# Kernel optimization log

Hardware: AMD Instinct MI355X
Metric: run time of the kernel (lower is better)

Reference implementation:

```python
import jax, jax.numpy as jnp
import numpy as np

MARGIN = 0.3
EPS = 1e-6  # torch pairwise_distance default eps used by TripletMarginLoss


def setup_inputs() -> dict:
    key = jax.random.key(0)
    k1, k2 = jax.random.split(key)
    emb = jax.random.normal(k1, (4096, 256), dtype=jnp.float32)
    emb = emb / jnp.linalg.norm(emb, axis=1, keepdims=True)  # docstring: normalized embeddings
    labels = jax.random.randint(k2, (4096,), 0, 64, dtype=jnp.int64) if jax.config.jax_enable_x64 else jax.random.randint(k2, (4096,), 0, 64, dtype=jnp.int32)
    return {"embeddings": emb, "labels": labels}


def _triplet_mining_loss(embeddings, labels):
    B = embeddings.shape[0]
    # pairwise euclidean distances via GEMM (matches torch.cdist p=2)
    sq = jnp.sum(embeddings * embeddings, axis=1)
    d2 = sq[:, None] + sq[None, :] - 2.0 * (embeddings @ embeddings.T)
    dist = jnp.sqrt(jnp.maximum(d2, 0.0))  # [B, B]

    same = labels[:, None] == labels[None, :]
    eye = jnp.eye(B, dtype=bool)
    pos_mask = same & ~eye
    neg_mask = ~same
    valid = pos_mask.any(axis=1) & neg_mask.any(axis=1)

    # hardest positive per anchor
    ap = jnp.where(pos_mask, dist, -jnp.inf)
    hp_idx = jnp.argmax(ap, axis=1)                           # [B]
    ap_dist = jnp.take_along_axis(dist, hp_idx[:, None], 1)[:, 0]

    # semi-hard negative: ap < d_an < ap + margin; pick FIRST such index (original takes semi_hard_indices[0])
    semi = neg_mask & (dist > ap_dist[:, None]) & (dist < ap_dist[:, None] + MARGIN)
    any_semi = semi.any(axis=1)
    first_semi = jnp.argmax(semi, axis=1)                     # argmax of bool = first True
    an = jnp.where(neg_mask, dist, jnp.inf)
    hardest_neg = jnp.argmin(an, axis=1)
    neg_idx = jnp.where(any_semi, first_semi, hardest_neg)

    # triplet margin loss recomputed from embeddings (torch adds EPS inside the norm)
    pos_e = embeddings[hp_idx]
    neg_e = embeddings[neg_idx]
    d_ap = jnp.linalg.norm(embeddings - pos_e + EPS, axis=1)
    d_an = jnp.linalg.norm(embeddings - neg_e + EPS, axis=1)
    per_anchor = jnp.maximum(d_ap - d_an + MARGIN, 0.0)

    vf = valid.astype(embeddings.dtype)
    cnt = jnp.sum(vf)
    return jnp.where(cnt > 0, jnp.sum(per_anchor * vf) / jnp.maximum(cnt, 1.0), 0.0)


def reference(embeddings, labels):
    return _triplet_mining_loss(embeddings, labels)
```

## Files before the change

### kernel.cpp

```cpp
#include <hip/hip_runtime.h>
#include <math.h>

#define BN 4096
#define DIM 256
#define D4 (DIM/4)
#define MI 8
#define MARGINF 0.3f
#define EPSF 1e-6f
#define SCAP 96
#define IMAX 0x7fffffff
#define PCAP 512

typedef __attribute__((ext_vector_type(8))) short bf16x8;
typedef __attribute__((ext_vector_type(4))) float f32x4;

__device__ __forceinline__ float fma4(float4 a, float4 b, float c){
  return fmaf(a.x,b.x, fmaf(a.y,b.y, fmaf(a.z,b.z, fmaf(a.w,b.w, c))));
}
__device__ __forceinline__ unsigned short f2bf(float x){
  unsigned u = __float_as_uint(x);
  return (unsigned short)((u + 0x7FFFu + ((u>>16)&1u)) >> 16);
}
__device__ __forceinline__ float bf2f(unsigned short h){
  return __uint_as_float(((unsigned)h)<<16);
}

__global__ __launch_bounds__(256) void k_pre2(const float* __restrict__ E,
     unsigned short* __restrict__ EhiT, unsigned short* __restrict__ EloT,
     float* __restrict__ sq, unsigned int* __restrict__ counter){
  int t = threadIdx.x;
  int g = blockIdx.x;
  const float4* E4 = (const float4*)E;
  bf16x8* HT = (bf16x8*)EhiT;
  bf16x8* LT = (bf16x8*)EloT;
  #pragma unroll
  for (int it=0; it<2; it++){
    int idx = it*256 + t;
    int kk = idx>>6, sub = idx&63, q = sub>>4, n = sub&15;
    int r = g*16 + n;
    int c = kk*4 + q;
    float4 v0 = E4[(size_t)r*64 + c*2];
    float4 v1 = E4[(size_t)r*64 + c*2 + 1];
    unsigned short h[8], lo[8];
    float vv[8] = {v0.x,v0.y,v0.z,v0.w, v1.x,v1.y,v1.z,v1.w};
    #pragma unroll
    for (int i=0;i<8;i++){ h[i]=f2bf(vv[i]); lo[i]=f2bf(vv[i]-bf2f(h[i])); }
    bf16x8 hv, lv;
    #pragma unroll
    for (int i=0;i<8;i++){ hv[i]=(short)h[i]; lv[i]=(short)lo[i]; }
    size_t d = (size_t)g*512 + idx;
    HT[d] = hv; LT[d] = lv;
  }
  int row = t>>4, part = t&15;
  const float4* rp = E4 + (size_t)(g*16+row)*64 + part*4;
  float s0 = fma4(rp[0],rp[0],0.f);
  float s1 = fma4(rp[1],rp[1],0.f);
  s0 = fma4(rp[2],rp[2],s0);
  s1 = fma4(rp[3],rp[3],s1);
  float s = s0+s1;
  s += __shfl_xor(s,1); s += __shfl_xor(s,2); s += __shfl_xor(s,4); s += __shfl_xor(s,8);
  if (part==0) sq[g*16+row] = s;
  if (g==0 && t==0) counter[0] = 0u;
}

__global__ __launch_bounds__(256) void k_posm(const float* __restrict__ E,
     const int* __restrict__ labels, const float* __restrict__ sq,
     float* __restrict__ apw, int* __restrict__ hpw,
     unsigned long long* __restrict__ negKey, unsigned int* __restrict__ semiJ){
  __shared__ __align__(16) int   labsS[BN];
  __shared__ __align__(16) float sqS[BN];
  __shared__ int mem[4][PCAP+4];
  int t=threadIdx.x, l=t&63, w=t>>6;
  #pragma unroll
  for (int i=0;i<4;i++){
    ((int4*)labsS)[i*256+t]   = ((const int4*)labels)[i*256+t];
    ((float4*)sqS)[i*256+t]   = ((const float4*)sq)[i*256+t];
  }
  __syncthreads();
  int aw = blockIdx.x*4 + w;
  int labW = labsS[aw];
  float sqw_ = sqS[aw];
  const float4* E4 = (const float4*)E;
  float4 areg = E4[(size_t)aw*64 + l];
  int cnt = 0;
  for (int c=0;c<64;c++){
    int j = c*64 + l;
    bool m = (labsS[j]==labW) && (j != aw);
    unsigned long long mask = __ballot(m);
    if (m){
      int pos = cnt + __popcll(mask & ((1ull<<l)-1ull));
      if (pos < PCAP) mem[w][pos] = j;
    }
    cnt += __popcll(mask);
  }
  if (cnt > PCAP) cnt = PCAP;
  if (l < 4) mem[w][cnt + l] = aw;
  float bv2 = -INFINITY; int bj = IMAX;
  for (int base=0; base<cnt; base+=4){
    int j0=mem[w][base+0], j1=mem[w][base+1], j2=mem[w][base+2], j3=mem[w][base+3];
    float4 r0=E4[(size_t)j0*64+l];
    float4 r1=E4[(size_t)j1*64+l];
    float4 r2=E4[(size_t)j2*64+l];
    float4 r3=E4[(size_t)j3*64+l];
    float p0=fma4(areg,r0,0.f), p1=fma4(areg,r1,0.f);
    float p2=fma4(areg,r2,0.f), p3=fma4(areg,r3,0.f);
    #pragma unroll
    for (int off=32; off; off>>=1){
      p0 += __shfl_xor(p0,off); p1 += __shfl_xor(p1,off);
      p2 += __shfl_xor(p2,off); p3 += __shfl_xor(p3,off);
    }
    float d0 = sqw_ + sqS[j0] - 2.0f*p0;
    float d1 = sqw_ + sqS[j1] - 2.0f*p1;
    float d2 = sqw_ + sqS[j2] - 2.0f*p2;
    float d3 = sqw_ + sqS[j3] - 2.0f*p3;
    if (d0 > bv2){ bv2=d0; bj=j0; }
    if (base+1<cnt && d1 > bv2){ bv2=d1; bj=j1; }
    if (base+2<cnt && d2 > bv2){ bv2=d2; bj=j2; }
    if (base+3<cnt && d3 > bv2){ bv2=d3; bj=j3; }
  }
  if (l==0){
    apw[aw] = (bj==IMAX) ? -INFINITY : sqrtf(fmaxf(bv2, 0.0f));
    hpw[aw] = (bj==IMAX) ? 0 : bj;
    negKey[aw] = ~0ull;
    semiJ[aw]  = 0xFFFFFFFFu;
  }
}

__global__ __launch_bounds__(1024,4) void k_negm(
     const unsigned short* __restrict__ EhiT, const unsigned short* __restrict__ EloT,
     const int* __restrict__ labels, const float* __restrict__ sq,
     const float* __restrict__ apw,
     unsigned long long* __restrict__ negKey, unsigned int* __restrict__ semiJ){
  __shared__ bf16x8 afH[1024];
  __shared__ bf16x8 afL[1024];
  __shared__ __align__(16) int   labsH[2048];
  __shared__ __align__(16) float sqH[2048];
  __shared__ float rnv[16][32]; __shared__ int rnj[16][32]; __shared__ int rsm[16][32];
  int t=threadIdx.x, l=t&63, w=t>>6;
  int lane16 = l&15, quad = l>>4;
  int q8   = blockIdx.x & 7;
  int half = q8 >> 2;
  int grp  = (blockIdx.x >> 3)*4 + (q8 & 3);
  int a0 = grp*32;
  int hbase = half*2048;
  const bf16x8* HT = (const bf16x8*)EhiT;
  const bf16x8* LT = (const bf16x8*)EloT;
  afH[t] = HT[(size_t)grp*1024 + t];
  afL[t] = LT[(size_t)grp*1024 + t];
  { int2   lv = ((const int2*)(labels + hbase))[t];
    labsH[2*t] = lv.x; labsH[2*t+1] = lv.y;
    float2 sv = ((const float2*)(sq + hbase))[t];
    sqH[2*t] = sv.x; sqH[2*t+1] = sv.y; }
  float sqa[2][4]; int laba[2][4]; float ap2[2][4]; float th2[2][4];
  #pragma unroll
  for (int g=0; g<2; g++){
    #pragma unroll
    for (int r=0; r<4; r++){
      int ag = a0 + g*16 + quad*4 + r;
      sqa[g][r] = sq[ag]; laba[g][r] = labels[ag];
      float ap = apw[ag];
      ap2[g][r] = ap*ap;
      float th = ap + MARGINF;
      th2[g][r] = th*th;
    }
  }
  __syncthreads();
  float mn[2][4]; int mj[2][4]; int sm[2][4];
  #pragma unroll
  for (int g=0; g<2; g++)
    #pragma unroll
    for (int r=0; r<4; r++){ mn[g][r]=INFINITY; mj[g][r]=IMAX; sm[g][r]=IMAX; }
  #pragma unroll 1
  for (int tile=0; tile<8; tile++){
    int gl = w*8 + tile;
    size_t BBase = (size_t)(half*128 + gl) * 512;
    f32x4 acc00={0.f,0.f,0.f,0.f}, acc01=acc00, acc02=acc00;
    f32x4 acc10=acc00, acc11=acc00, acc12=acc00;
    #pragma unroll 2
    for (int kk=0; kk<8; kk++){
      bf16x8 bh  = HT[BBase + kk*64 + l];
      bf16x8 bl  = LT[BBase + kk*64 + l];
      bf16x8 ah0 = afH[kk*64 + l];
      bf16x8 al0 = afL[kk*64 + l];
      bf16x8 ah1 = afH[512 + kk*64 + l];
      bf16x8 al1 = afL[512 + kk*64 + l];
      acc00 = __builtin_amdgcn_mfma_f32_16x16x32_bf16(ah0, bh, acc00, 0,0,0);
      acc01 = __builtin_amdgcn_mfma_f32_16x16x32_bf16(ah0, bl, acc01, 0,0,0);
      acc02 = __builtin_amdgcn_mfma_f32_16x16x32_bf16(al0, bh, acc02, 0,0,0);
      acc10 = __builtin_amdgcn_mfma_f32_16x16x32_bf16(ah1, bh, acc10, 0,0,0);
      acc11 = __builtin_amdgcn_mfma_f32_16x16x32_bf16(ah1, bl, acc11, 0,0,0);
      acc12 = __builtin_amdgcn_mfma_f32_16x16x32_bf16(al1, bh, acc12, 0,0,0);
    }
    int jloc = gl*16 + lane16;
    int lj = labsH[jloc]; float sqj = sqH[jloc];
    int jglob = hbase + jloc;
    #pragma unroll
    for (int r=0; r<4; r++){
      float dot0 = acc00[r] + (acc01[r] + acc02[r]);
      float d20  = sqa[0][r] + sqj - 2.0f*dot0;
      if (lj != laba[0][r]){
        if (d20 < mn[0][r]){ mn[0][r]=d20; mj[0][r]=jglob; }
        if (d20 > ap2[0][r] && d20 < th2[0][r] && jglob < sm[0][r]) sm[0][r]=jglob;
      }
      float dot1 = acc10[r] + (acc11[r] + acc12[r]);
      float d21  = sqa[1][r] + sqj - 2.0f*dot1;
      if (lj != laba[1][r]){
        if (d21 < mn[1][r]){ mn[1][r]=d21; mj[1][r]=jglob; }
        if (d21 > ap2[1][r] && d21 < th2[1][r] && jglob < sm[1][r]) sm[1][r]=jglob;
      }
    }
  }
  #pragma unroll
  for (int g=0; g<2; g++){
    #pragma unroll
    for (int r=0; r<4; r++){
      float v=mn[g][r]; int j=mj[g][r]; int s=sm[g][r];
      #pragma unroll
      for (int off=1; off<16; off<<=1){
        float v2=__shfl_xor(v,off); int j2=__shfl_xor(j,off); int s2=__shfl_xor(s,off);
        if (v2<v || (v2==v && j2<j)){ v=v2; j=j2; }
        s = (s2<s)?s2:s;
      }
      if (lane16==0){
        int ai = g*16 + quad*4 + r;
        rnv[w][ai]=v; rnj[w][ai]=j; rsm[w][ai]=s;
      }
    }
  }
  __syncthreads();
  if (t < 32){
    float V=INFINITY; int J=IMAX; int S=IMAX;
    for (int q=0; q<16; q++){
      float v2=rnv[q][t]; int j2=rnj[q][t];
      if (v2<V || (v2==V && j2<J)){ V=v2; J=j2; }
      int s2=rsm[q][t]; S=(s2<S)?s2:S;
    }
    unsigned u = __float_as_uint(V);
    unsigned key = (u & 0x80000000u) ? ~u : (u | 0x80000000u);
    unsigned long long k64 = (((unsigned long long)key)<<32) | (unsigned)J;
    atomicMin(&negKey[a0+t], k64);
    if (S != IMAX) atomicMin(&semiJ[a0+t], (unsigned)S);
  }
}

__global__ __launch_bounds__(256) void k_fin2(const float* __restrict__ E,
     const float* __restrict__ apw, const int* __restrict__ hpw,
     const unsigned long long* __restrict__ negKey, const unsigned int* __restrict__ semiJ,
     float* __restrict__ partials, unsigned int* __restrict__ counter,
     float* __restrict__ out){
  __shared__ float lsumS[4], lcntS[4];
  __shared__ float rs[4], rc[4];
  __shared__ int lastFlag;
  int t=threadIdx.x, l=t&63, w=t>>6;
  const float4* E4 = (const float4*)E;
  float lsum=0.f, lcnt=0.f;
  #pragma unroll 1
  for (int i=0;i<4;i++){
    int a = blockIdx.x*16 + w*4 + i;
    unsigned long long k64 = negKey[a];
    unsigned Jn = (unsigned)(k64 & 0xFFFFFFFFull);
    unsigned Sn = semiJ[a];
    bool anyneg = (Jn != (unsigned)IMAX);
    int ng = (Sn != 0xFFFFFFFFu) ? (int)Sn : (int)Jn;
    float ap = apw[a];
    bool dov = (ap != -INFINITY) && anyneg;
    if (dov){
      int hp = hpw[a];
      float4 av = E4[(size_t)a*64 + l];
      float4 pv = E4[(size_t)hp*64 + l];
      float4 nv = E4[(size_t)ng*64 + l];
      float d0=av.x-pv.x+EPSF, d1=av.y-pv.y+EPSF, d2=av.z-pv.z+EPSF, d3=av.w-pv.w+EPSF;
      float sp = fmaf(d0,d0, fmaf(d1,d1, fmaf(d2,d2, d3*d3)));
      float n0=av.x-nv.x+EPSF, n1=av.y-nv.y+EPSF, n2=av.z-nv.z+EPSF, n3=av.w-nv.w+EPSF;
      float sn = fmaf(n0,n0, fmaf(n1,n1, fmaf(n2,n2, n3*n3)));
      #pragma unroll
      for (int off=32; off; off>>=1){ sp += __shfl_xor(sp,off); sn += __shfl_xor(sn,off); }
      lsum += fmaxf(sqrtf(sp)-sqrtf(sn)+MARGINF, 0.0f);
      lcnt += 1.0f;
    }
  }
  if (l==0){ lsumS[w]=lsum; lcntS[w]=lcnt; }
  __syncthreads();
  if (t==0){
    partials[2*blockIdx.x]   = (lsumS[0]+lsumS[1])+(lsumS[2]+lsumS[3]);
    partials[2*blockIdx.x+1] = (lcntS[0]+lcntS[1])+(lcntS[2]+lcntS[3]);
    __threadfence();
    unsigned int old = atomicAdd(counter, 1u);
    lastFlag = (old == gridDim.x - 1) ? 1 : 0;
  }
  __syncthreads();
  if (lastFlag){
    __threadfence();
    float s = partials[2*t], c = partials[2*t+1];
    #pragma unroll
    for (int off=32; off; off>>=1){ s += __shfl_xor(s,off); c += __shfl_xor(c,off); }
    if (l==0){ rs[w]=s; rc[w]=c; }
    __syncthreads();
    if (t==0){
      float S=(rs[0]+rs[1])+(rs[2]+rs[3]);
      float C=(rc[0]+rc[1])+(rc[2]+rc[3]);
      out[0] = (C>0.0f) ? S/fmaxf(C,1.0f) : 0.0f;
    }
  }
}

__global__ __launch_bounds__(256) void k_sq(const float* __restrict__ E, float* __restrict__ sq){
  int i = blockIdx.x*256 + threadIdx.x;
  if (i >= BN) return;
  const float4* r = (const float4*)E + (size_t)i*D4;
  float a0=0.f,a1=0.f,a2=0.f,a3=0.f;
  #pragma unroll
  for (int q=0;q<D4;q+=4){
    a0 = fma4(r[q],r[q],a0);   a1 = fma4(r[q+1],r[q+1],a1);
    a2 = fma4(r[q+2],r[q+2],a2); a3 = fma4(r[q+3],r[q+3],a3);
  }
  sq[i] = (a0+a1)+(a2+a3);
}

__global__ __launch_bounds__(256) void k_pos(const float* __restrict__ E, const int* __restrict__ labels,
                       const float* __restrict__ sq, float* __restrict__ apw,
                       int* __restrict__ hpw, int* __restrict__ anypw){
  __shared__ int members[1024];
  __shared__ float4 mem4[SCAP*65];
  __shared__ int cnts[16][4];
  __shared__ int offs[16][4];
  __shared__ int cntS;
  int t = threadIdx.x, lane = t&63, w = t>>6;
  int c = blockIdx.x >> 2, split = blockIdx.x & 3;
  for (int ch=0; ch<16; ch++){
    bool m = (labels[ch*256 + t] == c);
    unsigned long long mask = __ballot(m);
    if (lane==0) cnts[ch][w] = __popcll(mask);
  }
  __syncthreads();
  if (t==0){
    int run=0;
    for (int ch=0; ch<16; ch++)
      for (int q=0;q<4;q++){ offs[ch][q]=run; run+=cnts[ch][q]; }
    cntS = run;
  }
  __syncthreads();
  int cnt = cntS; if (cnt>1024) cnt=1024;
  for (int ch=0; ch<16; ch++){
    int idx = ch*256 + t;
    bool m = (labels[idx] == c);
    unsigned long long mask = __ballot(m);
    int my = __popcll(mask & ((1ull<<lane)-1ull));
    int pos = offs[ch][w] + my;
    if (m && pos < 1024) members[pos] = idx;
  }
  int S = (cnt < SCAP) ? cnt : SCAP;
  int anyp = (cnt >= 2) ? 1 : 0;
  __syncthreads();
  const float4* E4 = (const float4*)E;
  for (int idx=t; idx<S*64; idx+=256){
    int row = idx>>6, f = idx&63;
    mem4[row*65 + f] = E4[(size_t)members[row]*D4 + f];
  }
  __syncthreads();
  int esplit = split*4 + w;
  int p = lane&3, cand = lane>>2;
  int passes = (cnt+15)>>4;
  for (int mi=esplit; mi<cnt; mi+=16){
    int i = members[mi];
    float sqi = sq[i];
    float4 ai4[16];
    if (mi < S){
      #pragma unroll
      for (int m=0;m<16;m++) ai4[m] = mem4[mi*65 + p + 4*m];
    } else {
      #pragma unroll
      for (int m=0;m<16;m++) ai4[m] = E4[(size_t)i*D4 + p + 4*m];
    }
    float bv = -INFINITY; int bj = IMAX;
    for (int ps=0; ps<passes; ps++){
      int mj = ps*16 + cand;
      if (mj < cnt && mj != mi){
        int j = members[mj];
        float a0v=0.f, a1v=0.f;
        if (mj < S){
          const float4* rj = mem4 + mj*65 + p;
          #pragma unroll
          for (int m=0;m<16;m+=2){ a0v=fma4(ai4[m],rj[4*m],a0v); a1v=fma4(ai4[m+1],rj[4*(m+1)],a1v); }
        } else {
          const float4* rj = E4 + (size_t)j*D4 + p;
          #pragma unroll
          for (int m=0;m<16;m+=2){ a0v=fma4(ai4[m],rj[4*m],a0v); a1v=fma4(ai4[m+1],rj[4*(m+1)],a1v); }
        }
        float acc = a0v+a1v;
        acc += __shfl_xor(acc,1); acc += __shfl_xor(acc,2);
        float d = sqrtf(fmaxf(sqi + sq[j] - 2.0f*acc, 0.0f));
        if (p==0){ if (d > bv || (d==bv && j<bj)){ bv=d; bj=j; } }
      }
    }
    #pragma unroll
    for (int off=32; off; off>>=1){
      float v2=__shfl_xor(bv,off); int j2=__shfl_xor(bj,off);
      if (v2>bv || (v2==bv && j2<bj)){ bv=v2; bj=j2; }
    }
    if (lane==0){
      int J = (bj==IMAX) ? 0 : bj;
      apw[i]=bv; hpw[i]=J; anypw[i]=anyp;
    }
  }
}

__global__ __launch_bounds__(256,2) void k_main(const float* __restrict__ E, const int* __restrict__ labels,
     const float* __restrict__ sq, const float* __restrict__ apw, const int* __restrict__ hpw,
     const int* __restrict__ anypw, float* __restrict__ partials){
  __shared__ float4 At[MI*68 + 4];
  __shared__ float redv[4][MI]; __shared__ int redj[4][MI]; __shared__ int redsm[4][MI];
  __shared__ int finNeg[MI]; __shared__ int finVal[MI];
  __shared__ float redp[4], redn[4];
  int t=threadIdx.x, lane=t&63, w=t>>6;
  int a0 = blockIdx.x * MI;
  const float4* E4 = (const float4*)E;
  for (int idx=t; idx<MI*64; idx+=256){
    int a=idx>>6, q=idx&63, pp=q&3, mm=q>>2;
    At[a*68 + pp*17 + mm] = E4[(size_t)(a0+a)*D4 + q];
  }
  __syncthreads();
  float apv[MI], sqi[MI]; int labi[MI];
  #pragma unroll
  for (int a=0;a<MI;a++){ apv[a]=apw[a0+a]; sqi[a]=sq[a0+a]; labi[a]=labels[a0+a]; }
  float mnv[MI]; int mnj[MI]; int smj[MI];
  #pragma unroll
  for (int a=0;a<MI;a++){ mnv[a]=INFINITY; mnj[a]=0; smj[a]=IMAX; }
  int s = t>>2, p = t&3;
  for (int it=0; it<16; it++){
    int colb = it*256 + 4*s;
    const float4* __restrict__ bp = E4 + (size_t)colb*D4 + p;
    float acc[MI][4];
    #pragma unroll
    for (int a=0;a<MI;a++){
      #pragma unroll
      for (int c2=0;c2<4;c2++) acc[a][c2]=0.0f;
    }
    for (int mg=0; mg<4; mg++){
      float4 b[4][4];
      #pragma unroll
      for (int c2=0;c2<4;c2++){
        #pragma unroll
        for (int m=0;m<4;m++) b[m][c2] = bp[(size_t)c2*D4 + mg*16 + m*4];
      }
      #pragma unroll
      for (int a=0;a<MI;a++){
        float4 a4[4];
        #pragma unroll
        for (int m=0;m<4;m++) a4[m] = At[a*68 + p*17 + mg*4 + m];
        #pragma unroll
        for (int m=0;m<4;m++){
          #pragma unroll
          for (int c2=0;c2<4;c2++) acc[a][c2] = fma4(a4[m], b[m][c2], acc[a][c2]);
        }
      }
    }
    #pragma unroll
    for (int a=0;a<MI;a++){
      #pragma unroll
      for (int c2=0;c2<4;c2++){
        float v = acc[a][c2];
        v += __shfl_xor(v,1); v += __shfl_xor(v,2);
        acc[a][c2] = v;
      }
    }
    #pragma unroll
    for (int c2=0;c2<4;c2++){
      int j = colb + c2;
      int lj = labels[j]; float sqj = sq[j];
      #pragma unroll
      for (int a=0;a<MI;a++){
        float d = sqrtf(fmaxf(sqi[a]+sqj-2.0f*acc[a][c2], 0.0f));
        if (lj != labi[a]){
          if (d < mnv[a]){ mnv[a]=d; mnj[a]=j; }
          if (d > apv[a] && d < apv[a]+MARGINF && j < smj[a]) smj[a]=j;
        }
      }
    }
  }
  #pragma unroll
  for (int a=0;a<MI;a++){
    float v=mnv[a]; int j=mnj[a]; int sm=smj[a];
    #pragma unroll
    for (int off=32; off; off>>=1){
      float v2=__shfl_xor(v,off); int j2=__shfl_xor(j,off); int s2=__shfl_xor(sm,off);
      if (v2<v || (v2==v && j2<j)){ v=v2; j=j2; }
      sm = (s2<sm)?s2:sm;
    }
    if (lane==0){ redv[w][a]=v; redj[w][a]=j; redsm[w][a]=sm; }
  }
  __syncthreads();
  if (t < MI){
    int a=t;
    float V=INFINITY; int J=0; int S=IMAX; bool first=true;
    for (int q=0;q<4;q++){
      float v2=redv[q][a]; int j2=redj[q][a];
      if (first || v2<V || (v2==V && j2<J)){ V=v2; J=j2; first=false; }
      int s2=redsm[q][a]; S=(s2<S)?s2:S;
    }
    bool anyneg = (V < INFINITY);
    finNeg[a] = (S != IMAX) ? S : J;
    finVal[a] = (anypw[a0+a] != 0 && anyneg) ? 1 : 0;
  }
  __syncthreads();
  float lsum=0.0f, lcnt=0.0f;
  for (int a=0;a<MI;a++){
    if (finVal[a]){
      int hp = hpw[a0+a]; int ng = finNeg[a];
      float ai = E[(size_t)(a0+a)*DIM + t];
      float pv = E[(size_t)hp*DIM + t];
      float nv = E[(size_t)ng*DIM + t];
      float dp = ai - pv + EPSF; float dn = ai - nv + EPSF;
      float sp = dp*dp, sn = dn*dn;
      #pragma unroll
      for (int off=32; off; off>>=1){ sp += __shfl_xor(sp,off); sn += __shfl_xor(sn,off); }
      if (lane==0){ redp[w]=sp; redn[w]=sn; }
    }
    __syncthreads();
    if (finVal[a] && t==0){
      float SP=(redp[0]+redp[1])+(redp[2]+redp[3]);
      float SN=(redn[0]+redn[1])+(redn[2]+redn[3]);
      lsum += fmaxf(sqrtf(SP)-sqrtf(SN)+MARGINF, 0.0f);
      lcnt += 1.0f;
    }
    __syncthreads();
  }
  if (t==0){ partials[2*blockIdx.x]=lsum; partials[2*blockIdx.x+1]=lcnt; }
}

__global__ __launch_bounds__(256) void k_fin(const float* __restrict__ partials, float* __restrict__ out, int nb){
  __shared__ float rs[4], rc[4];
  int t=threadIdx.x, lane=t&63, w=t>>6;
  float s=0.f, c=0.f;
  for (int q=t;q<nb;q+=256){ s+=partials[2*q]; c+=partials[2*q+1]; }
  #pragma unroll
  for (int off=32; off; off>>=1){ s+=__shfl_xor(s,off); c+=__shfl_xor(c,off); }
  if (lane==0){ rs[w]=s; rc[w]=c; }
  __syncthreads();
  if (t==0){
    float S=(rs[0]+rs[1])+(rs[2]+rs[3]);
    float C=(rc[0]+rc[1])+(rc[2]+rc[3]);
    out[0] = (C>0.0f) ? S/fmaxf(C,1.0f) : 0.0f;
  }
}

extern "C" void kernel_launch(void* const* d_in, const int* in_sizes, int n_in,
                              void* d_out, int out_size, void* d_ws, size_t ws_size,
                              hipStream_t stream) {
  const float* E      = (const float*)d_in[0];
  const int*   labels = (const int*)d_in[1];
  float* out = (float*)d_out;

  float* sqw      = (float*)d_ws;
  float* apw      = sqw + BN;
  int*   hpw      = (int*)(apw + BN);
  int*   anypw    = hpw + BN;
  float* partials = (float*)(anypw + BN);
  unsigned int* counter = (unsigned int*)(partials + 1024);
  unsigned long long* negKey = (unsigned long long*)((char*)d_ws + 72*1024);
  unsigned int*       semiJ  = (unsigned int*)((char*)d_ws + 104*1024);
  unsigned short* EhiT = (unsigned short*)((char*)d_ws + 131072);
  unsigned short* EloT = EhiT + (size_t)BN*DIM;
  bool big = ws_size >= (size_t)(131072 + 4*1024*1024);

  if (big){
    k_pre2<<<256,  256,  0, stream>>>(E, EhiT, EloT, sqw, counter);
    k_posm<<<1024, 256,  0, stream>>>(E, labels, sqw, apw, hpw, negKey, semiJ);
    k_negm<<<256,  1024, 0, stream>>>(EhiT, EloT, labels, sqw, apw, negKey, semiJ);
    k_fin2<<<256,  256,  0, stream>>>(E, apw, hpw, negKey, semiJ, partials, counter, out);
  } else {
    k_sq  <<<BN/256, 256, 0, stream>>>(E, sqw);
    k_pos <<<256,    256, 0, stream>>>(E, labels, sqw, apw, hpw, anypw);
    k_main<<<BN/MI,  256, 0, stream>>>(E, labels, sqw, apw, hpw, anypw, partials);
    k_fin <<<1,      256, 0, stream>>>(partials, out, BN/MI);
  }
}
```

Before: 152.0 us.

## Split positive mining across 8 candidates per wave and quarter negative mining columns

k_posm stops staging all labels and squared norms in LDS. Each wave now evaluates 8 positive candidates at once, with 8 lanes per candidate holding the anchor row in registers, and the 64-lane shuffle reduction becomes a 3-step reduce followed by a cross-group argmax. The positive capacity drops from 512 to 192. k_negm splits the column range into quarters instead of halves and launches 512 blocks, so each block runs 4 tiles and gets more parallelism. The tighter positive cap could truncate positive lists on other label distributions, and the negative-side merge logic must handle four splits.

```diff
diff --git a/kernel.cpp b/kernel.cpp
--- a/kernel.cpp
+++ b/kernel.cpp
@@ -9,7 +9,7 @@
 #define EPSF 1e-6f
 #define SCAP 96
 #define IMAX 0x7fffffff
-#define PCAP 512
+#define PCAP2 192
 
 typedef __attribute__((ext_vector_type(8))) short bf16x8;
 typedef __attribute__((ext_vector_type(4))) float f32x4;
@@ -63,60 +63,51 @@
   if (g==0 && t==0) counter[0] = 0u;
 }
 
-__global__ __launch_bounds__(256) void k_posm(const float* __restrict__ E,
+__global__ __launch_bounds__(256,4) void k_posm(const float* __restrict__ E,
      const int* __restrict__ labels, const float* __restrict__ sq,
      float* __restrict__ apw, int* __restrict__ hpw,
      unsigned long long* __restrict__ negKey, unsigned int* __restrict__ semiJ){
-  __shared__ __align__(16) int   labsS[BN];
-  __shared__ __align__(16) float sqS[BN];
-  __shared__ int mem[4][PCAP+4];
+  __shared__ int mem[4][PCAP2+16];
   int t=threadIdx.x, l=t&63, w=t>>6;
-  #pragma unroll
-  for (int i=0;i<4;i++){
-    ((int4*)labsS)[i*256+t]   = ((const int4*)labels)[i*256+t];
-    ((float4*)sqS)[i*256+t]   = ((const float4*)sq)[i*256+t];
-  }
-  __syncthreads();
   int aw = blockIdx.x*4 + w;
-  int labW = labsS[aw];
-  float sqw_ = sqS[aw];
+  int labW = labels[aw];
+  float sqa = sq[aw];
   const float4* E4 = (const float4*)E;
-  float4 areg = E4[(size_t)aw*64 + l];
+  int p = l&7, cand = l>>3;
+  float4 ai4[8];
+  #pragma unroll
+  for (int m=0;m<8;m++) ai4[m] = E4[(size_t)aw*64 + p*8 + m];
   int cnt = 0;
+  #pragma unroll 4
   for (int c=0;c<64;c++){
     int j = c*64 + l;
-    bool m = (labsS[j]==labW) && (j != aw);
+    bool m = (labels[j]==labW) && (j != aw);
     unsigned long long mask = __ballot(m);
     if (m){
       int pos = cnt + __popcll(mask & ((1ull<<l)-1ull));
-      if (pos < PCAP) mem[w][pos] = j;
+      if (pos < PCAP2) mem[w][pos] = j;
     }
     cnt += __popcll(mask);
   }
-  if (cnt > PCAP) cnt = PCAP;
-  if (l < 4) mem[w][cnt + l] = aw;
+  if (cnt > PCAP2) cnt = PCAP2;
+  if (l < 16) mem[w][cnt + l] = aw;
   float bv2 = -INFINITY; int bj = IMAX;
-  for (int base=0; base<cnt; base+=4){
-    int j0=mem[w][base+0], j1=mem[w][base+1], j2=mem[w][base+2], j3=mem[w][base+3];
-    float4 r0=E4[(size_t)j0*64+l];
-    float4 r1=E4[(size_t)j1*64+l];
-    float4 r2=E4[(size_t)j2*64+l];
-    float4 r3=E4[(size_t)j3*64+l];
-    float p0=fma4(areg,r0,0.f), p1=fma4(areg,r1,0.f);
-    float p2=fma4(areg,r2,0.f), p3=fma4(areg,r3,0.f);
-    #pragma unroll
-    for (int off=32; off; off>>=1){
-      p0 += __shfl_xor(p0,off); p1 += __shfl_xor(p1,off);
-      p2 += __shfl_xor(p2,off); p3 += __shfl_xor(p3,off);
-    }
-    float d0 = sqw_ + sqS[j0] - 2.0f*p0;
-    float d1 = sqw_ + sqS[j1] - 2.0f*p1;
-    float d2 = sqw_ + sqS[j2] - 2.0f*p2;
-    float d3 = sqw_ + sqS[j3] - 2.0f*p3;
-    if (d0 > bv2){ bv2=d0; bj=j0; }
-    if (base+1<cnt && d1 > bv2){ bv2=d1; bj=j1; }
-    if (base+2<cnt && d2 > bv2){ bv2=d2; bj=j2; }
-    if (base+3<cnt && d3 > bv2){ bv2=d3; bj=j3; }
+  for (int base=0; base<cnt; base+=8){
+    int ci = base + cand;
+    int j = mem[w][ci];
+    const float4* rj = E4 + (size_t)j*64 + p*8;
+    float sqj = sq[j];
+    float acc = fma4(ai4[0], rj[0], 0.f);
+    #pragma unroll
+    for (int m=1;m<8;m++) acc = fma4(ai4[m], rj[m], acc);
+    acc += __shfl_xor(acc,1); acc += __shfl_xor(acc,2); acc += __shfl_xor(acc,4);
+    float d2 = sqa + sqj - 2.0f*acc;
+    if (ci < cnt && d2 > bv2){ bv2 = d2; bj = j; }
+  }
+  #pragma unroll
+  for (int off=8; off<64; off<<=1){
+    float v2=__shfl_xor(bv2,off); int j2=__shfl_xor(bj,off);
+    if (v2>bv2 || (v2==bv2 && j2<bj)){ bv2=v2; bj=j2; }
   }
   if (l==0){
     apw[aw] = (bj==IMAX) ? -INFINITY : sqrtf(fmaxf(bv2, 0.0f));
@@ -133,24 +124,22 @@
      unsigned long long* __restrict__ negKey, unsigned int* __restrict__ semiJ){
   __shared__ bf16x8 afH[1024];
   __shared__ bf16x8 afL[1024];
-  __shared__ __align__(16) int   labsH[2048];
-  __shared__ __align__(16) float sqH[2048];
+  __shared__ __align__(16) int   labsH[1024];
+  __shared__ __align__(16) float sqH[1024];
   __shared__ float rnv[16][32]; __shared__ int rnj[16][32]; __shared__ int rsm[16][32];
   int t=threadIdx.x, l=t&63, w=t>>6;
   int lane16 = l&15, quad = l>>4;
-  int q8   = blockIdx.x & 7;
-  int half = q8 >> 2;
-  int grp  = (blockIdx.x >> 3)*4 + (q8 & 3);
+  int q8    = blockIdx.x & 7;
+  int split = q8 >> 1;
+  int grp   = (blockIdx.x >> 3)*2 + (q8 & 1);
   int a0 = grp*32;
-  int hbase = half*2048;
+  int hbase = split*1024;
   const bf16x8* HT = (const bf16x8*)EhiT;
   const bf16x8* LT = (const bf16x8*)EloT;
   afH[t] = HT[(size_t)grp*1024 + t];
   afL[t] = LT[(size_t)grp*1024 + t];
-  { int2   lv = ((const int2*)(labels + hbase))[t];
-    labsH[2*t] = lv.x; labsH[2*t+1] = lv.y;
-    float2 sv = ((const float2*)(sq + hbase))[t];
-    sqH[2*t] = sv.x; sqH[2*t+1] = sv.y; }
+  labsH[t] = labels[hbase + t];
+  sqH[t]   = sq[hbase + t];
   float sqa[2][4]; int laba[2][4]; float ap2[2][4]; float th2[2][4];
   #pragma unroll
   for (int g=0; g<2; g++){
@@ -171,9 +160,9 @@
     #pragma unroll
     for (int r=0; r<4; r++){ mn[g][r]=INFINITY; mj[g][r]=IMAX; sm[g][r]=IMAX; }
   #pragma unroll 1
-  for (int tile=0; tile<8; tile++){
-    int gl = w*8 + tile;
-    size_t BBase = (size_t)(half*128 + gl) * 512;
+  for (int tile=0; tile<4; tile++){
+    int gl = w*4 + tile;
+    size_t BBase = (size_t)(split*64 + gl) * 512;
     f32x4 acc00={0.f,0.f,0.f,0.f}, acc01=acc00, acc02=acc00;
     f32x4 acc10=acc00, acc11=acc00, acc12=acc00;
     #pragma unroll 2
@@ -566,7 +555,7 @@
   if (big){
     k_pre2<<<256,  256,  0, stream>>>(E, EhiT, EloT, sqw, counter);
     k_posm<<<1024, 256,  0, stream>>>(E, labels, sqw, apw, hpw, negKey, semiJ);
-    k_negm<<<256,  1024, 0, stream>>>(EhiT, EloT, labels, sqw, apw, negKey, semiJ);
+    k_negm<<<512,  1024, 0, stream>>>(EhiT, EloT, labels, sqw, apw, negKey, semiJ);
     k_fin2<<<256,  256,  0, stream>>>(E, apw, hpw, negKey, semiJ, partials, counter, out);
   } else {
     k_sq  <<<BN/256, 256, 0, stream>>>(E, sqw);
```

Result: slower. 198.4 us (+30.5%).
